# Kernel tuning notes

Hardware: AMD Instinct MI355X
Metric: run time of the kernel (lower is better)

The kernel has to match this reference:

```python
import jax, jax.numpy as jnp
import numpy as np

# Standard NF4 quantization levels (bitsandbytes / QLoRA)
NF4_LEVELS = jnp.array([
    -1.0, -0.6961928009986877, -0.5250730514526367, -0.39491748809814453,
    -0.28444138169288635, -0.18477343022823334, -0.09105003625154495, 0.0,
    0.07958029955625534, 0.16093020141124725, 0.24611230194568634,
    0.33791524171829224, 0.44070982933044434, 0.5626170039176941,
    0.7229568362236023, 1.0], dtype=jnp.float32)

D_IN, D_OUT = 4096, 4096
BLOCK_SIZE = 64
N_VALS = D_IN * D_OUT              # 16_777_216 weights
N_BYTES = N_VALS // 2              # 2 nibbles per byte
NUM_BLOCKS = N_VALS // BLOCK_SIZE  # 262_144 per-block scales


def setup_inputs() -> dict:
    key = jax.random.key(0)
    k1, k2, k3, k4 = jax.random.split(key, 4)
    x = jax.random.normal(k1, (4, 2048, D_IN), dtype=jnp.float32)
    kernel_quantized = jax.random.randint(k2, (N_BYTES,), 0, 256, dtype=jnp.int32)
    kernel_scales = jax.random.uniform(k3, (NUM_BLOCKS,), dtype=jnp.float32)
    bias = jax.random.normal(k4, (D_OUT,), dtype=jnp.float32)
    return {"x": x, "kernel_quantized": kernel_quantized,
            "kernel_scales": kernel_scales, "bias": bias}


def nf4_dequantize(kernel_quantized, kernel_scales):
    # Unpack two 4-bit codes per byte (high nibble first), look up NF4 level,
    # scale per block of BLOCK_SIZE values, reshape to original kernel shape.
    high = (kernel_quantized >> 4) & 0xF
    low = kernel_quantized & 0xF
    codes = jnp.stack([high, low], axis=-1).reshape(-1)          # [N_VALS]
    vals = NF4_LEVELS[codes]                                     # [N_VALS]
    vals = vals.reshape(NUM_BLOCKS, BLOCK_SIZE) * kernel_scales[:, None]
    return vals.reshape(D_IN, D_OUT)                             # pad_length = 0


def reference(x, kernel_quantized, kernel_scales, bias):
    # Dense base-layer call on the dequantized kernel: x @ W + b
    W = nf4_dequantize(kernel_quantized, kernel_scales)
    out = jnp.einsum('bsd,de->bse', x, W) + bias
    return out.astype(jnp.float32)
```

## Files before the change

### kernel.cpp

```cpp
#include <hip/hip_runtime.h>
#include <hip/hip_bf16.h>
#include <stdint.h>

typedef __bf16 bf16x8 __attribute__((ext_vector_type(8)));
typedef float f32x4 __attribute__((ext_vector_type(4)));
typedef float f32x16 __attribute__((ext_vector_type(16)));
typedef unsigned short ushort_t;
typedef ushort_t ushort8 __attribute__((ext_vector_type(8)));

#define GLDS16(g, l) __builtin_amdgcn_global_load_lds(                          \
    (const __attribute__((address_space(1))) void*)(g),                         \
    (__attribute__((address_space(3))) void*)(l), 16, 0, 0)

__device__ __constant__ float NF4_LUT_C[16] = {
    -1.0f, -0.6961928009986877f, -0.5250730514526367f, -0.39491748809814453f,
    -0.28444138169288635f, -0.18477343022823334f, -0.09105003625154495f, 0.0f,
    0.07958029955625534f, 0.16093020141124725f, 0.24611230194568634f,
    0.33791524171829224f, 0.44070982933044434f, 0.5626170039176941f,
    0.7229568362236023f, 1.0f};

__device__ inline ushort_t f32_to_bf16(float f) {
    uint32_t u = __builtin_bit_cast(uint32_t, f);
    u += 0x7FFFu + ((u >> 16) & 1u);
    return (ushort_t)(u >> 16);
}

__global__ __launch_bounds__(256) void cast_x_kernel(
    const float* __restrict__ x, ushort_t* __restrict__ xb)
{
    const int i = blockIdx.x * 256 + threadIdx.x;
    const float4* p = reinterpret_cast<const float4*>(x);
    float4 a = p[i * 2];
    float4 b = p[i * 2 + 1];
    ushort8 v;
    v[0] = f32_to_bf16(a.x); v[1] = f32_to_bf16(a.y);
    v[2] = f32_to_bf16(a.z); v[3] = f32_to_bf16(a.w);
    v[4] = f32_to_bf16(b.x); v[5] = f32_to_bf16(b.y);
    v[6] = f32_to_bf16(b.z); v[7] = f32_to_bf16(b.w);
    *reinterpret_cast<ushort8*>(xb + (size_t)i * 8) = v;
}

__global__ __launch_bounds__(256) void nf4_dequant_t_kernel(
    const int* __restrict__ q, const float* __restrict__ scales,
    ushort_t* __restrict__ Wt)
{
    __shared__ float lut[16];
    __shared__ ushort_t tile[64][65];
    const int t = threadIdx.x;
    if (t < 16) lut[t] = NF4_LUT_C[t];
    __syncthreads();

    const int nt = blockIdx.x & 63;
    const int kt = blockIdx.x >> 6;

    #pragma unroll
    for (int L = t; L < 512; L += 256) {
        const int r  = L >> 3;
        const int qd = L & 7;
        const int k  = kt * 64 + r;
        const int4 e4 = *reinterpret_cast<const int4*>(q + (size_t)k * 2048 + nt * 32 + qd * 4);
        const float s = scales[k * 64 + nt];
        const int nb = qd * 8;
        int bts[4] = {e4.x, e4.y, e4.z, e4.w};
        #pragma unroll
        for (int e = 0; e < 4; ++e) {
            const int byte = bts[e];
            tile[r][nb + e * 2]     = f32_to_bf16(lut[(byte >> 4) & 0xF] * s);
            tile[r][nb + e * 2 + 1] = f32_to_bf16(lut[byte & 0xF] * s);
        }
    }
    __syncthreads();

    const int nl = t >> 2;
    const int ks = (t & 3) * 16;
    ushort8 v0, v1;
    #pragma unroll
    for (int j = 0; j < 8; ++j) v0[j] = tile[ks + j][nl];
    #pragma unroll
    for (int j = 0; j < 8; ++j) v1[j] = tile[ks + 8 + j][nl];
    ushort_t* dst = Wt + (size_t)(nt * 64 + nl) * 4096 + kt * 64 + ks;
    *reinterpret_cast<ushort8*>(dst)     = v0;
    *reinterpret_cast<ushort8*>(dst + 8) = v1;
}

__global__ __launch_bounds__(512, 2) void gemm_nf4_kernel(
    const ushort_t* __restrict__ A, const ushort_t* __restrict__ Bt,
    const float* __restrict__ bias, float* __restrict__ C)
{
    __shared__ __align__(16) ushort_t As[4][256 * 32];
    __shared__ __align__(16) ushort_t Bs[4][256 * 32];

    const int tid  = threadIdx.x;
    const int lane = tid & 63;
    const int wid  = tid >> 6;
    const int wr   = wid >> 2;
    const int wc   = wid & 3;
    const int ln31 = lane & 31;
    const int lq2  = lane >> 5;
    const int ln2  = (lane >> 1) & 3;

    const int wg  = blockIdx.x;
    const int swz = (wg & 7) * 64 + (wg >> 3);
    const int m0  = (swz >> 4) * 256;
    const int n0  = (swz & 15) * 256;

    const int srow = wid * 16 + (lane >> 2);
    const int scol = ((lane & 3) ^ ((lane >> 3) & 3)) * 8;
    const ushort_t* gA0 = A  + (size_t)(m0 + srow) * 4096 + scol;
    const ushort_t* gA1 = gA0 + (size_t)128 * 4096;
    const ushort_t* gB0 = Bt + (size_t)(n0 + srow) * 4096 + scol;
    const ushort_t* gB1 = gB0 + (size_t)128 * 4096;
    const int ldsOff0 = (wid * 16) * 32;
    const int ldsOff1 = (128 + wid * 16) * 32;

    f32x16 acc[4][2];
    #pragma unroll
    for (int i = 0; i < 4; ++i)
        #pragma unroll
        for (int j = 0; j < 2; ++j)
            acc[i][j] = (f32x16){0.f};

    const int po0 = ((0 * 2 + lq2) ^ ln2) << 3;
    const int po1 = ((1 * 2 + lq2) ^ ln2) << 3;
    const int rdA = (wr * 128 + ln31) * 32;
    const int rdB = (wc * 64  + ln31) * 32;

    #pragma unroll
    for (int tt = 0; tt < 3; ++tt) {
        const int kof = tt * 32;
        GLDS16(gA0 + kof, &As[tt][ldsOff0]);
        GLDS16(gA1 + kof, &As[tt][ldsOff1]);
        GLDS16(gB0 + kof, &Bs[tt][ldsOff0]);
        GLDS16(gB1 + kof, &Bs[tt][ldsOff1]);
    }
    asm volatile("s_waitcnt vmcnt(8)" ::: "memory");
    __builtin_amdgcn_s_barrier();
    __builtin_amdgcn_sched_barrier(0);

    for (int t = 0; t < 128; ++t) {
        const int slot = t & 3;
        const ushort_t* Asl = &As[slot][0];
        const ushort_t* Bsl = &Bs[slot][0];
        const int nslot = (t + 3) & 3;
        const int kof   = (t + 3) * 32;

        bf16x8 bf0[2], af0[4], bf1[2], af1[4];
        #pragma unroll
        for (int j = 0; j < 2; ++j)
            bf0[j] = *reinterpret_cast<const bf16x8*>(Bsl + rdB + j * 32 * 32 + po0);
        #pragma unroll
        for (int i = 0; i < 4; ++i)
            af0[i] = *reinterpret_cast<const bf16x8*>(Asl + rdA + i * 32 * 32 + po0);
        if (t < 125) {
            GLDS16(gA0 + kof, &As[nslot][ldsOff0]);
            GLDS16(gA1 + kof, &As[nslot][ldsOff1]);
        }
        __builtin_amdgcn_s_setprio(1);
        #pragma unroll
        for (int i = 0; i < 4; ++i)
            #pragma unroll
            for (int j = 0; j < 2; ++j)
                acc[i][j] = __builtin_amdgcn_mfma_f32_32x32x16_bf16(
                    af0[i], bf0[j], acc[i][j], 0, 0, 0);
        __builtin_amdgcn_s_setprio(0);

        #pragma unroll
        for (int j = 0; j < 2; ++j)
            bf1[j] = *reinterpret_cast<const bf16x8*>(Bsl + rdB + j * 32 * 32 + po1);
        #pragma unroll
        for (int i = 0; i < 4; ++i)
            af1[i] = *reinterpret_cast<const bf16x8*>(Asl + rdA + i * 32 * 32 + po1);
        if (t < 125) {
            GLDS16(gB0 + kof, &Bs[nslot][ldsOff0]);
            GLDS16(gB1 + kof, &Bs[nslot][ldsOff1]);
        }
        __builtin_amdgcn_s_setprio(1);
        #pragma unroll
        for (int i = 0; i < 4; ++i)
            #pragma unroll
            for (int j = 0; j < 2; ++j)
                acc[i][j] = __builtin_amdgcn_mfma_f32_32x32x16_bf16(
                    af1[i], bf1[j], acc[i][j], 0, 0, 0);
        __builtin_amdgcn_s_setprio(0);

        if (t < 125)       asm volatile("s_waitcnt vmcnt(8)" ::: "memory");
        else if (t == 125) asm volatile("s_waitcnt vmcnt(4)" ::: "memory");
        else if (t == 126) asm volatile("s_waitcnt vmcnt(0)" ::: "memory");
        __builtin_amdgcn_s_barrier();
        __builtin_amdgcn_sched_barrier(0);
    }

    const int crow_b = m0 + wr * 128 + lq2 * 4;
    const int ccol_b = n0 + wc * 64 + ln31;
    #pragma unroll
    for (int j = 0; j < 2; ++j) {
        const int c = ccol_b + j * 32;
        const float bv = bias[c];
        #pragma unroll
        for (int i = 0; i < 4; ++i) {
            #pragma unroll
            for (int reg = 0; reg < 16; ++reg) {
                const int r = crow_b + i * 32 + (reg & 3) + 8 * (reg >> 2);
                C[(size_t)r * 4096 + c] = acc[i][j][reg] + bv;
            }
        }
    }
}

extern "C" void kernel_launch(void* const* d_in, const int* in_sizes, int n_in,
                              void* d_out, int out_size, void* d_ws, size_t ws_size,
                              hipStream_t stream) {
    const float* x      = (const float*)d_in[0];
    const int*   q      = (const int*)d_in[1];
    const float* scales = (const float*)d_in[2];
    const float* bias   = (const float*)d_in[3];
    float* out = (float*)d_out;

    ushort_t* xb = (ushort_t*)d_ws;
    ushort_t* Wt = (ushort_t*)((char*)d_ws + (size_t)64 * 1024 * 1024);

    cast_x_kernel<<<16384, 256, 0, stream>>>(x, xb);
    nf4_dequant_t_kernel<<<4096, 256, 0, stream>>>(q, scales, Wt);
    gemm_nf4_kernel<<<512, 512, 0, stream>>>(xb, Wt, bias, out);
}
```

Measured before the change: 325.8 us.

## Switch GEMM to double-buffered BK=64 with MFMA-fragment-ordered LDS layout

Reworks the GEMM main loop from a 4-stage BK=32 ring buffer to a 2-stage BK=64 double buffer. Global-to-LDS loads now write each 16-byte chunk straight into the MFMA operand fragment order, so every lane reads its fragment at lane*8 with no XOR swizzle and no bank conflicts. This halves the number of barriers per K and simplifies addressing. In exchange prefetch depth drops to one stage and each iteration waits on vmcnt(0), which can expose global load latency.

```diff
diff --git a/kernel.cpp b/kernel.cpp
--- a/kernel.cpp
+++ b/kernel.cpp
@@ -3,7 +3,6 @@
 #include <stdint.h>
 
 typedef __bf16 bf16x8 __attribute__((ext_vector_type(8)));
-typedef float f32x4 __attribute__((ext_vector_type(4)));
 typedef float f32x16 __attribute__((ext_vector_type(16)));
 typedef unsigned short ushort_t;
 typedef ushort_t ushort8 __attribute__((ext_vector_type(8)));
@@ -87,31 +86,24 @@
     const ushort_t* __restrict__ A, const ushort_t* __restrict__ Bt,
     const float* __restrict__ bias, float* __restrict__ C)
 {
-    __shared__ __align__(16) ushort_t As[4][256 * 32];
-    __shared__ __align__(16) ushort_t Bs[4][256 * 32];
+    __shared__ __align__(16) ushort_t As[2][16384];
+    __shared__ __align__(16) ushort_t Bs[2][16384];
 
     const int tid  = threadIdx.x;
     const int lane = tid & 63;
-    const int wid  = tid >> 6;
-    const int wr   = wid >> 2;
-    const int wc   = wid & 3;
+    const int w8   = tid >> 6;
+    const int wr   = w8 >> 2;
+    const int wc   = w8 & 3;
     const int ln31 = lane & 31;
     const int lq2  = lane >> 5;
-    const int ln2  = (lane >> 1) & 3;
 
     const int wg  = blockIdx.x;
     const int swz = (wg & 7) * 64 + (wg >> 3);
     const int m0  = (swz >> 4) * 256;
     const int n0  = (swz & 15) * 256;
 
-    const int srow = wid * 16 + (lane >> 2);
-    const int scol = ((lane & 3) ^ ((lane >> 3) & 3)) * 8;
-    const ushort_t* gA0 = A  + (size_t)(m0 + srow) * 4096 + scol;
-    const ushort_t* gA1 = gA0 + (size_t)128 * 4096;
-    const ushort_t* gB0 = Bt + (size_t)(n0 + srow) * 4096 + scol;
-    const ushort_t* gB1 = gB0 + (size_t)128 * 4096;
-    const int ldsOff0 = (wid * 16) * 32;
-    const int ldsOff1 = (128 + wid * 16) * 32;
+    const ushort_t* gA = A  + (size_t)(m0 + w8 * 32 + ln31) * 4096 + lq2 * 8;
+    const ushort_t* gB = Bt + (size_t)(n0 + w8 * 32 + ln31) * 4096 + lq2 * 8;
 
     f32x16 acc[4][2];
     #pragma unroll
@@ -120,72 +112,52 @@
         for (int j = 0; j < 2; ++j)
             acc[i][j] = (f32x16){0.f};
 
-    const int po0 = ((0 * 2 + lq2) ^ ln2) << 3;
-    const int po1 = ((1 * 2 + lq2) ^ ln2) << 3;
-    const int rdA = (wr * 128 + ln31) * 32;
-    const int rdB = (wc * 64  + ln31) * 32;
+    const int aBase = wr * 8192 + lane * 8;
+    const int bBase = wc * 4096 + lane * 8;
 
     #pragma unroll
-    for (int tt = 0; tt < 3; ++tt) {
-        const int kof = tt * 32;
-        GLDS16(gA0 + kof, &As[tt][ldsOff0]);
-        GLDS16(gA1 + kof, &As[tt][ldsOff1]);
-        GLDS16(gB0 + kof, &Bs[tt][ldsOff0]);
-        GLDS16(gB1 + kof, &Bs[tt][ldsOff1]);
+    for (int q = 0; q < 4; ++q) {
+        GLDS16(gA + q * 16, &As[0][(w8 * 4 + q) * 512]);
+        GLDS16(gB + q * 16, &Bs[0][(w8 * 4 + q) * 512]);
     }
-    asm volatile("s_waitcnt vmcnt(8)" ::: "memory");
+    asm volatile("s_waitcnt vmcnt(0)" ::: "memory");
     __builtin_amdgcn_s_barrier();
     __builtin_amdgcn_sched_barrier(0);
 
-    for (int t = 0; t < 128; ++t) {
-        const int slot = t & 3;
-        const ushort_t* Asl = &As[slot][0];
-        const ushort_t* Bsl = &Bs[slot][0];
-        const int nslot = (t + 3) & 3;
-        const int kof   = (t + 3) * 32;
+    for (int t = 0; t < 64; ++t) {
+        const int p = t & 1;
 
-        bf16x8 bf0[2], af0[4], bf1[2], af1[4];
+        if (t < 63) {
+            const int kof = (t + 1) * 64;
+            #pragma unroll
+            for (int q = 0; q < 4; ++q) {
+                GLDS16(gA + kof + q * 16, &As[p ^ 1][(w8 * 4 + q) * 512]);
+                GLDS16(gB + kof + q * 16, &Bs[p ^ 1][(w8 * 4 + q) * 512]);
+            }
+        }
+
+        const ushort_t* Ab = &As[p][aBase];
+        const ushort_t* Bb = &Bs[p][bBase];
         #pragma unroll
-        for (int j = 0; j < 2; ++j)
-            bf0[j] = *reinterpret_cast<const bf16x8*>(Bsl + rdB + j * 32 * 32 + po0);
-        #pragma unroll
-        for (int i = 0; i < 4; ++i)
-            af0[i] = *reinterpret_cast<const bf16x8*>(Asl + rdA + i * 32 * 32 + po0);
-        if (t < 125) {
-            GLDS16(gA0 + kof, &As[nslot][ldsOff0]);
-            GLDS16(gA1 + kof, &As[nslot][ldsOff1]);
-        }
-        __builtin_amdgcn_s_setprio(1);
-        #pragma unroll
-        for (int i = 0; i < 4; ++i)
+        for (int kk = 0; kk < 4; ++kk) {
+            bf16x8 af[4], bf[2];
+            #pragma unroll
+            for (int i = 0; i < 4; ++i)
+                af[i] = *reinterpret_cast<const bf16x8*>(Ab + (i * 4 + kk) * 512);
             #pragma unroll
             for (int j = 0; j < 2; ++j)
-                acc[i][j] = __builtin_amdgcn_mfma_f32_32x32x16_bf16(
-                    af0[i], bf0[j], acc[i][j], 0, 0, 0);
-        __builtin_amdgcn_s_setprio(0);
+                bf[j] = *reinterpret_cast<const bf16x8*>(Bb + (j * 4 + kk) * 512);
+            __builtin_amdgcn_s_setprio(1);
+            #pragma unroll
+            for (int i = 0; i < 4; ++i)
+                #pragma unroll
+                for (int j = 0; j < 2; ++j)
+                    acc[i][j] = __builtin_amdgcn_mfma_f32_32x32x16_bf16(
+                        af[i], bf[j], acc[i][j], 0, 0, 0);
+            __builtin_amdgcn_s_setprio(0);
+        }
 
-        #pragma unroll
-        for (int j = 0; j < 2; ++j)
-            bf1[j] = *reinterpret_cast<const bf16x8*>(Bsl + rdB + j * 32 * 32 + po1);
-        #pragma unroll
-        for (int i = 0; i < 4; ++i)
-            af1[i] = *reinterpret_cast<const bf16x8*>(Asl + rdA + i * 32 * 32 + po1);
-        if (t < 125) {
-            GLDS16(gB0 + kof, &Bs[nslot][ldsOff0]);
-            GLDS16(gB1 + kof, &Bs[nslot][ldsOff1]);
-        }
-        __builtin_amdgcn_s_setprio(1);
-        #pragma unroll
-        for (int i = 0; i < 4; ++i)
-            #pragma unroll
-            for (int j = 0; j < 2; ++j)
-                acc[i][j] = __builtin_amdgcn_mfma_f32_32x32x16_bf16(
-                    af1[i], bf1[j], acc[i][j], 0, 0, 0);
-        __builtin_amdgcn_s_setprio(0);
-
-        if (t < 125)       asm volatile("s_waitcnt vmcnt(8)" ::: "memory");
-        else if (t == 125) asm volatile("s_waitcnt vmcnt(4)" ::: "memory");
-        else if (t == 126) asm volatile("s_waitcnt vmcnt(0)" ::: "memory");
+        if (t < 63) asm volatile("s_waitcnt vmcnt(0)" ::: "memory");
         __builtin_amdgcn_s_barrier();
         __builtin_amdgcn_sched_barrier(0);
     }
```

Result: slower. 440.1 us (+35.1%).
